# Kernel tuning notes

Hardware: AMD Instinct MI355X
Metric: run time of the kernel (lower is better)

## Reference

```python
import jax, jax.numpy as jnp
import numpy as np

WAY = 5
TEMPERATURE = 0.2
TEMPERATURE_ATTN = 5.0
BN_EPS = 1e-5


def bn_apply(x, p):
    # p: (4, C) = gamma, beta, running_mean, running_var (eval-mode BatchNorm)
    g, b, m, v = p[0], p[1], p[2], p[3]
    sh = (1, -1) + (1,) * (x.ndim - 2)
    return (x - m.reshape(sh)) * (g.reshape(sh) / jnp.sqrt(v.reshape(sh) + BN_EPS)) + b.reshape(sh)


def conv3d(x, w, pad):
    return jax.lax.conv_general_dilated(
        x, w, (1, 1, 1), [(pad[0], pad[0]), (pad[1], pad[1]), (pad[2], pad[2])],
        dimension_numbers=('NCDHW', 'OIDHW', 'NCDHW'))


def sepconv4d(x, conv2_w, bn2, conv1_w, bn1, proj_w, bnp):
    # x: (b, c, u, v, h, w). conv2: (k,k,1) kernel over (u,v); conv1: (1,k,k) over (h,w).
    b, c, u, v, h, w = x.shape
    y = x.reshape(b, c, u, v, h * w)
    y = bn_apply(conv3d(y, conv2_w, (1, 1, 0)), bn2)
    y = jax.nn.relu(y)
    y = y.reshape(b, c, u * v, h, w)
    y = bn_apply(conv3d(y, conv1_w, (0, 1, 1)), bn1)
    # 1x1 projection (pointwise over channels) + BN
    y = jnp.einsum('oc,bcxhw->boxhw', proj_w, y)
    y = bn_apply(y, bnp)
    return y.reshape(b, -1, u, v, h, w)


def cca(x, c1, c2):
    def branch(z):
        z = sepconv4d(z, *c1)
        z = jax.nn.relu(z)
        z = sepconv4d(z, *c2)
        return z
    perm = (0, 1, 4, 5, 2, 3)
    return branch(x) + jnp.transpose(branch(jnp.transpose(x, perm)), perm)


def gaussian_normalize(x, axis, eps=1e-5):
    m = jnp.mean(x, axis=axis, keepdims=True)
    v = jnp.var(x, axis=axis, keepdims=True, ddof=1)  # torch.var is unbiased
    return (x - m) / jnp.sqrt(v + eps)


def setup_inputs() -> dict:
    key = jax.random.key(0)
    ks = jax.random.split(key, 16)

    def bn_params(k, c):
        k1, k2, k3, k4 = jax.random.split(k, 4)
        g = 1.0 + 0.1 * jax.random.normal(k1, (c,), jnp.float32)
        b = 0.1 * jax.random.normal(k2, (c,), jnp.float32)
        m = 0.1 * jax.random.normal(k3, (c,), jnp.float32)
        v = 1.0 + 0.1 * jax.random.uniform(k4, (c,), jnp.float32)
        return jnp.stack([g, b, m, v])

    return {
        'spt': jax.random.normal(ks[0], (1, 5, 640, 10, 10), jnp.float32),
        'qry': jax.random.normal(ks[1], (75, 640, 10, 10), jnp.float32),
        'w_1x1': jax.random.normal(ks[2], (64, 640), jnp.float32) * 0.04,
        'bn_1x1': bn_params(ks[3], 64),
        'c1_conv2_w': jax.random.normal(ks[4], (1, 1, 3, 3, 1), jnp.float32) * 0.33,
        'c1_bn2': bn_params(ks[5], 1),
        'c1_conv1_w': jax.random.normal(ks[6], (1, 1, 1, 3, 3), jnp.float32) * 0.33,
        'c1_bn1': bn_params(ks[7], 1),
        'c1_proj_w': jax.random.normal(ks[8], (16, 1), jnp.float32),
        'c1_bnp': bn_params(ks[9], 16),
        'c2_conv2_w': jax.random.normal(ks[10], (16, 16, 3, 3, 1), jnp.float32) * 0.083,
        'c2_bn2': bn_params(ks[11], 16),
        'c2_conv1_w': jax.random.normal(ks[12], (16, 16, 1, 3, 3), jnp.float32) * 0.083,
        'c2_bn1': bn_params(ks[13], 16),
        'c2_proj_w': jax.random.normal(ks[14], (1, 16), jnp.float32) * 0.25,
        'c2_bnp': bn_params(ks[15], 1),
    }


def reference(spt, qry, w_1x1, bn_1x1,
              c1_conv2_w, c1_bn2, c1_conv1_w, c1_bn1, c1_proj_w, c1_bnp,
              c2_conv2_w, c2_bn2, c2_conv1_w, c2_bn1, c2_proj_w, c2_bnp):
    s = spt[0]                                   # (way, C, H, W)
    s = s - s.mean(axis=1, keepdims=True)        # normalize_feature
    q = qry - qry.mean(axis=1, keepdims=True)

    def cca1x1(x):
        y = jnp.einsum('oc,bchw->bohw', w_1x1, x)
        return jax.nn.relu(bn_apply(y, bn_1x1))

    sf = cca1x1(s)
    qf = cca1x1(q)
    sf = sf / jnp.maximum(jnp.linalg.norm(sf, axis=1, keepdims=True), 1e-8)
    qf = qf / jnp.maximum(jnp.linalg.norm(qf, axis=1, keepdims=True), 1e-8)

    # 4D correlation (avoids the repeat-induced 6D blowup of the original)
    corr = jnp.einsum('ncij,qckl->qnijkl', sf, qf)  # (Q, way, Hs, Ws, Hq, Wq)
    Q, way, Hs, Ws, Hq, Wq = corr.shape

    c1 = (c1_conv2_w, c1_bn2, c1_conv1_w, c1_bn1, c1_proj_w, c1_bnp)
    c2 = (c2_conv2_w, c2_bn2, c2_conv1_w, c2_bn1, c2_proj_w, c2_bnp)
    corr = cca(corr.reshape(Q * way, 1, Hs, Ws, Hq, Wq), c1, c2)

    corr_s = corr.reshape(Q, way, Hs * Ws, Hq, Wq)
    corr_q = corr.reshape(Q, way, Hs, Ws, Hq * Wq)
    corr_s = gaussian_normalize(corr_s, axis=2)
    corr_q = gaussian_normalize(corr_q, axis=4)
    corr_s = jax.nn.softmax(corr_s / TEMPERATURE_ATTN, axis=2).reshape(Q, way, Hs, Ws, Hq, Wq)
    corr_q = jax.nn.softmax(corr_q / TEMPERATURE_ATTN, axis=4).reshape(Q, way, Hs, Ws, Hq, Wq)

    attn_s = corr_s.sum(axis=(4, 5))             # (Q, way, Hs, Ws)
    attn_q = corr_q.sum(axis=(2, 3))             # (Q, way, Hq, Wq)

    spt_att = (attn_s[:, :, None] * s[None]).mean(axis=(-1, -2))       # (Q, way, C)
    qry_att = (attn_q[:, :, None] * q[:, None]).mean(axis=(-1, -2))    # (Q, way, C)
    qry_pooled = q.mean(axis=(-1, -2))                                  # (Q, C)

    num = jnp.sum(spt_att * qry_att, axis=-1)
    den = (jnp.maximum(jnp.linalg.norm(spt_att, axis=-1), 1e-8) *
           jnp.maximum(jnp.linalg.norm(qry_att, axis=-1), 1e-8))
    sim = (num / den) / TEMPERATURE
    return sim, qry_pooled
```

## Files before the change

### kernel.cpp

```cpp
#include <hip/hip_runtime.h>


#define NITEM 375

#define OFF_XTS 0
#define OFF_XTQ 160000
#define OFF_MP  2560000
#define OFF_SF  2568000
#define OFF_QF  2600000
#define OFF_RA  3080000
#define OFF_RB  6830000
#define OFF_PRM 10655000

#define PK2F 232
#define PK1F 1512
#define WSUMF 2792
#define SCVF 2856
#define SHVF 2920
#define PKWF 2984

#define Y1SLOT0  23680
#define Y1GAP3   3200
#define Y1SSTR3  35200
#define ZPB3     20480
#define Y2S3     129280
#define LDS_TOTAL3 161536

typedef float f4v __attribute__((ext_vector_type(4)));
typedef float f32x4 __attribute__((ext_vector_type(4)));
typedef _Float16 half8v __attribute__((ext_vector_type(8)));
typedef __fp16 fp16x2 __attribute__((ext_vector_type(2)));
typedef unsigned int u32x4 __attribute__((ext_vector_type(4)));
typedef unsigned int u32x2 __attribute__((ext_vector_type(2)));

__device__ __forceinline__ unsigned int pkrtz(float a, float b) {
  union { fp16x2 h; unsigned int u; } cv;
  cv.h = __builtin_amdgcn_cvt_pkrtz(a, b);
  return cv.u;
}

__global__ __launch_bounds__(256) void k_prep(
    const float* __restrict__ w1x1,  const float* __restrict__ bn1x1,
    const float* __restrict__ c1c2w, const float* __restrict__ c1bn2,
    const float* __restrict__ c1c1w, const float* __restrict__ c1bn1,
    const float* __restrict__ c1pj,  const float* __restrict__ c1bnp,
    const float* __restrict__ c2c2w, const float* __restrict__ c2bn2,
    const float* __restrict__ c2c1w, const float* __restrict__ c2bn1,
    const float* __restrict__ c2pj,  const float* __restrict__ c2bnp,
    float* __restrict__ prm)
{
  (void)w1x1; (void)bn1x1;
  const int t = threadIdx.x;
  const float eps = 1e-5f;

  for (int idx = t; idx < 144; idx += 256) {
    int ds = idx / 16, i = idx % 16;
    float spv = c2bnp[0] / sqrtf(c2bnp[3] + eps);
    float acc = 0.f;
    for (int o = 0; o < 16; ++o) {
      float s1 = c2bn1[o] / sqrtf(c2bn1[48 + o] + eps);
      acc += c2pj[o] * s1 * c2c1w[(o * 16 + i) * 9 + ds];
    }
    prm[idx] = spv * acc;
  }
  for (int i = t; i < 16; i += 256) {
    float s = c1bnp[i] / sqrtf(c1bnp[48 + i] + eps);
    prm[144 + i] = s * c1pj[i];
    prm[160 + i] = c1bnp[16 + i] - c1bnp[32 + i] * s;
  }
  for (int o = t; o < 16; o += 256) {
    float s = c2bn2[o] / sqrtf(c2bn2[48 + o] + eps);
    prm[176 + o] = s;
    prm[192 + o] = c2bn2[16 + o] - c2bn2[32 + o] * s;
  }
  for (int k = t; k < 9; k += 256) {
    prm[208 + k] = c1c2w[k];
    prm[217 + k] = c1c1w[k];
  }
  if (t == 0) {
    float S2 = c1bn2[0] / sqrtf(c1bn2[3] + eps);
    prm[226] = S2;
    prm[227] = c1bn2[1] - c1bn2[2] * S2;
    float S1 = c1bn1[0] / sqrtf(c1bn1[3] + eps);
    prm[228] = S1;
    prm[229] = c1bn1[1] - c1bn1[2] * S1;
    float spv = c2bnp[0] / sqrtf(c2bnp[3] + eps);
    float k0 = 0.f;
    for (int o = 0; o < 16; ++o) {
      float s1 = c2bn1[o] / sqrtf(c2bn1[48 + o] + eps);
      k0 += c2pj[o] * (c2bn1[16 + o] - c2bn1[32 + o] * s1);
    }
    prm[230] = spv * (k0 - c2bnp[2]) + c2bnp[1];
    prm[231] = 0.f;
  }
  __syncthreads();

  _Float16* pk2 = (_Float16*)(prm + PK2F);
  for (int idx = t; idx < 2560; idx += 256) {
    int c = idx >> 9, rem = idx & 511;
    int ln = rem >> 3, j = rem & 7;
    int o = ln & 15, qq = ln >> 4;
    int tap = 2 * c + (qq >> 1);
    int i = (qq & 1) * 8 + j;
    float v = (tap < 9) ? c2c2w[(o * 16 + i) * 9 + tap] : 0.f;
    pk2[idx] = (_Float16)v;
  }
  _Float16* pk1 = (_Float16*)(prm + PK1F);
  for (int idx = t; idx < 2560; idx += 256) {
    int c = idx >> 9, rem = idx & 511;
    int ln = rem >> 3, j = rem & 7;
    int m = ln & 15, qq = ln >> 4;
    int k = c * 32 + qq * 8 + j;
    int tp = k >> 4, i = k & 15;
    float v = (m == 0 && tp < 9) ? prm[tp * 16 + i] : 0.f;
    pk1[idx] = (_Float16)v;
  }
}

__global__ __launch_bounds__(256) void k_prepw(
    const float* __restrict__ w1x1, const float* __restrict__ bn1x1,
    float* __restrict__ prm)
{
  __shared__ float red[4];
  _Float16* pkw = (_Float16*)(prm + PKWF);
  const int t = threadIdx.x;
  const int base = blockIdx.x * 800;
  for (int r = t; r < 800; r += 256) {
    int idx = base + r;
    int fi = idx >> 9, rem = idx & 511;
    int ln = rem >> 3, j = rem & 7;
    int cc = fi / 10, r2 = fi - cc * 10;
    int mt = r2 >> 1, kk = r2 & 1;
    int m = mt * 16 + (ln & 15);
    int k = cc * 64 + kk * 32 + ((ln >> 4) & 3) * 8 + j;
    float v = (m < 64) ? w1x1[m * 640 + k] : (m == 64 ? 1.f : 0.f);
    pkw[idx] = (_Float16)v;
  }
  const int o = blockIdx.x;
  float s = 0.f;
  for (int c = t; c < 640; c += 256) s += w1x1[o * 640 + c];
  #pragma unroll
  for (int off = 32; off > 0; off >>= 1) s += __shfl_down(s, off);
  if ((t & 63) == 0) red[t >> 6] = s;
  __syncthreads();
  if (t == 0) {
    prm[WSUMF + o] = red[0] + red[1] + red[2] + red[3];
    float scv = bn1x1[o] / sqrtf(bn1x1[192 + o] + 1e-5f);
    prm[SCVF + o] = scv;
    prm[SHVF + o] = bn1x1[64 + o] - bn1x1[128 + o] * scv;
  }
}

__global__ __launch_bounds__(512) void k_feat(
    const float* __restrict__ spt, const float* __restrict__ qry,
    float* __restrict__ ws, float* __restrict__ out)
{
  __shared__ __align__(16) char POOL[2 * 16128];
  __shared__ __align__(16) float mrow[112];
  __shared__ __align__(16) float rn[112];
  __shared__ float CS[2][512];
  __shared__ float RS[640];
  __shared__ float msumL;

  const int b = blockIdx.x, t = threadIdx.x;
  const int lane = t & 63, wvv = t >> 6;
  const int n0 = lane & 15, qd = (lane >> 4) & 3;
  const float* src = (b < 5) ? spt + b * 64000 : qry + (b - 5) * 64000;
  float* dst = (b < 5) ? ws + OFF_SF + b * 6400 : ws + OFF_QF + (b - 5) * 6400;
  unsigned int* xtg = (unsigned int*)(ws + ((b < 5) ? (OFF_XTS + b * 32000)
                                                    : (OFF_XTQ + (b - 5) * 32000)));
  const float* prm = ws + OFF_PRM;
  const _Float16* pkw = (const _Float16*)(prm + PKWF);

  for (int idx = t; idx < 864; idx += 512) {
    int bsel = idx / 432, r = idx - bsel * 432;
    ((unsigned int*)(POOL + bsel * 16128 + 100 * 144))[r] = 0u;
  }
  for (int u = t; u < 800; u += 512) {
    int cp = u / 25, p4 = u - cp * 25;
    const float* r0 = src + (2 * cp) * 100 + p4 * 4;
    f4v a = *(const f4v*)r0;
    f4v c1 = *(const f4v*)(r0 + 100);
    #pragma unroll
    for (int e = 0; e < 4; ++e)
      *(unsigned int*)((_Float16*)POOL + (p4 * 4 + e) * 72 + 2 * cp) = pkrtz(a[e], c1[e]);
  }
  __syncthreads();

  const int chp = t >> 3, part = t & 7;
  const int pLo = part * 13, pHi = (pLo + 13 < 100) ? pLo + 13 : 100;

  f32x4 acc[5];
  #pragma unroll
  for (int ti = 0; ti < 5; ++ti) { acc[ti][0]=0.f; acc[ti][1]=0.f; acc[ti][2]=0.f; acc[ti][3]=0.f; }

  for (int cc = 0; cc < 10; ++cc) {
    const int cur = cc & 1;
    const _Float16* Xc = (const _Float16*)(POOL + cur * 16128);
    _Float16* Xn = (_Float16*)(POOL + (cur ^ 1) * 16128);

    f4v pa[2], pc[2];
    if (cc < 9) {
      #pragma unroll
      for (int k = 0; k < 2; ++k) {
        int u = t + k * 512;
        if (u < 800) {
          int cp = u / 25, p4 = u - cp * 25;
          const float* r0 = src + ((cc + 1) * 64 + 2 * cp) * 100 + p4 * 4;
          pa[k] = *(const f4v*)r0;
          pc[k] = *(const f4v*)(r0 + 100);
        }
      }
    }
    for (int u = t; u < 3200; u += 512) {
      int p = u >> 5, cp = u & 31;
      xtg[p * 320 + cc * 32 + cp] = *(const unsigned int*)(Xc + p * 72 + 2 * cp);
    }
    #pragma unroll
    for (int kk = 0; kk < 2; ++kk) {
      #pragma unroll
      for (int ti = 0; ti < 5; ++ti) {
        int idx = wvv + ti * 8; if (idx > 34) idx = 34;
        int mt = idx / 7, nt = idx - mt * 7;
        half8v av = *(const half8v*)(pkw + (cc * 10 + mt * 2 + kk) * 512 + lane * 8);
        half8v bv = *(const half8v*)(Xc + (nt * 16 + n0) * 72 + kk * 32 + qd * 8);
        acc[ti] = __builtin_amdgcn_mfma_f32_16x16x32_f16(av, bv, acc[ti], 0, 0, 0);
      }
    }
    {
      float s = 0.f;
      for (int p = pLo; p < pHi; ++p) s += (float)Xc[p * 72 + chp];
      CS[cur][t] = s;
    }
    if (cc < 9) {
      #pragma unroll
      for (int k = 0; k < 2; ++k) {
        int u = t + k * 512;
        if (u < 800) {
          int cp = u / 25, p4 = u - cp * 25;
          #pragma unroll
          for (int e = 0; e < 4; ++e)
            *(unsigned int*)(Xn + (p4 * 4 + e) * 72 + 2 * cp) = pkrtz(pa[k][e], pc[k][e]);
        }
      }
    }
    __syncthreads();
    if (t < 64) {
      float s = 0.f;
      #pragma unroll
      for (int k = 0; k < 8; ++k) s += CS[cur][t * 8 + k];
      RS[cc * 64 + t] = s;
    }
  }
  #pragma unroll
  for (int ti = 0; ti < 5; ++ti) {
    int idx = wvv + ti * 8; if (idx > 34) idx = 34;
    int mt = idx / 7, nt = idx - mt * 7;
    if (mt == 4 && qd == 0) {
      int p = nt * 16 + n0;
      mrow[p] = acc[ti][0] * (1.f / 640.f);
    }
  }
  __syncthreads();
  float* OUT = (float*)POOL;
  if (t == 0) { float s = 0.f; for (int p = 0; p < 100; ++p) s += mrow[p]; msumL = s; }
  #pragma unroll
  for (int ti = 0; ti < 5; ++ti) {
    int idx = wvv + ti * 8; if (idx > 34) idx = 34;
    int mt = idx / 7, nt = idx - mt * 7;
    if (mt < 4) {
      int p = nt * 16 + n0;
      if (p < 100) {
        float mp = mrow[p];
        #pragma unroll
        for (int r = 0; r < 4; ++r) {
          int o = mt * 16 + qd * 4 + r;
          float v = acc[ti][r] - prm[WSUMF + o] * mp;
          v = prm[SCVF + o] * v + prm[SHVF + o];
          OUT[o * 104 + p] = v > 0.f ? v : 0.f;
        }
      }
    }
  }
  __syncthreads();
  if (t < 100) {
    float s = 0.f;
    for (int o = 0; o < 64; ++o) { float v = OUT[o * 104 + t]; s += v * v; }
    float nr = sqrtf(s);
    rn[t] = 1.f / (nr > 1e-8f ? nr : 1e-8f);
    ws[OFF_MP + b * 100 + t] = mrow[t];
  }
  __syncthreads();
  for (int idx = t; idx < 1600; idx += 512) {
    int o = idx / 25, pq = idx - o * 25;
    f4v v = *(const f4v*)(OUT + o * 104 + pq * 4);
    f4v r4 = *(const f4v*)(rn + pq * 4);
    #pragma unroll
    for (int e = 0; e < 4; ++e) v[e] *= r4[e];
    *(f4v*)(dst + o * 100 + pq * 4) = v;
  }
  if (b >= 5) {
    const float msum = msumL;
    for (int gc = t; gc < 640; gc += 512)
      out[375 + (b - 5) * 640 + gc] = (RS[gc] - msum) * 0.01f;
  }
}

__global__ __launch_bounds__(1024) __attribute__((amdgpu_waves_per_eu(4, 4)))
void k_cca(float* __restrict__ ws)
{
  extern __shared__ char smem[];
  _Float16* T2h = (_Float16*)smem;
  float* sfL  = (float*)(smem + 20480);
  float* qfL  = (float*)(smem + 46080);
  float* CORR = (float*)(smem + 71680);
  float* T1   = (float*)(smem + 20480);

  const float* prm = ws + OFF_PRM;
  const int bid = blockIdx.x;
  const int it = bid >> 1, br = bid & 1;
  const int q = it / 5, n = it % 5;
  const int t = threadIdx.x;
  const int lane = t & 63, wv = t >> 6;
  const int n0 = lane & 15, qd = (lane >> 4) & 3;
  const int qh = qd >> 1, ih = qd & 1;

  const _Float16* pk2 = (const _Float16*)(prm + PK2F);
  const _Float16* pk1 = (const _Float16*)(prm + PK1F);
  half8v A2[5], A1[5];
  #pragma unroll
  for (int c = 0; c < 5; ++c) {
    A2[c] = *(const half8v*)(pk2 + c * 512 + lane * 8);
    A1[c] = *(const half8v*)(pk1 + c * 512 + lane * 8);
  }
  float sc2[4], bc2[4];
  #pragma unroll
  for (int r = 0; r < 4; ++r) { sc2[r] = prm[176 + qd * 4 + r]; bc2[r] = prm[192 + qd * 4 + r]; }

  const int d1E[5] = {-1,-1, 0, 0, 1}, d2E[5] = {-1, 1, 0,-1, 1};
  const int d1O[5] = {-1, 0, 0, 1, 0}, d2O[5] = { 0,-1, 1, 0, 0};

  int pp1[4], st1[4], addr2[4][5], posB[4];
  bool pv[4];
  #pragma unroll
  for (int ti = 0; ti < 4; ++ti) {
    int tile = wv + ti * 16; if (tile > 62) tile = 62;
    const int p = tile * 16 + n0;
    const int pcp = p < 1000 ? p : 999;
    pp1[ti] = pcp * 32 + ih * 16;
    st1[ti] = Y2S3 + p * 32 + qh * 16 + ih * 8;
    pv[ti] = (qd == 0) && (p < 1000);
    const int f2 = pcp / 100;
    const int s = pcp - f2 * 100;
    const int s1 = s / 10, s2 = s - s1 * 10;
    const bool rm = s1 > 0, rp = s1 < 9, cm = s2 > 0, cp2 = s2 < 9;
    const int b0 = Y2S3 + pcp * 32 + ih * 16;
    #pragma unroll
    for (int c = 0; c < 5; ++c) {
      const bool vE = (d1E[c] < 0 ? rm : (d1E[c] > 0 ? rp : true)) &&
                      (d2E[c] < 0 ? cm : (d2E[c] > 0 ? cp2 : true));
      const bool vO = (c == 4) ? false :
                      ((d1O[c] < 0 ? rm : (d1O[c] > 0 ? rp : true)) &&
                       (d2O[c] < 0 ? cm : (d2O[c] > 0 ? cp2 : true)));
      const bool v = qh ? vO : vE;
      const int D1c = (qh ? (d1O[c] * 10 + d2O[c]) : (d1E[c] * 10 + d2E[c]));
      addr2[ti][c] = v ? (b0 + D1c * 32) : ZPB3;
    }
    posB[ti] = br ? (s * 100 + f2) : (f2 * 100 + s);
  }
  const int posStride = br ? 10 : 1000;

  {
    const f4v* sf4 = (const f4v*)(ws + OFF_SF + n * 6400);
    const f4v* qf4 = (const f4v*)(ws + OFF_QF + q * 6400);
    f4v* sL4 = (f4v*)sfL; f4v* qL4 = (f4v*)qfL;
    for (int idx = t; idx < 1600; idx += 1024) { sL4[idx] = sf4[idx]; qL4[idx] = qf4[idx]; }
  }
  __syncthreads();

  if (t < 625) {
    const int ij0 = (t / 25) * 4, kl0 = (t % 25) * 4;
    f4v acc4[4];
    #pragma unroll
    for (int jj = 0; jj < 4; ++jj) { acc4[jj][0]=0.f; acc4[jj][1]=0.f; acc4[jj][2]=0.f; acc4[jj][3]=0.f; }
    for (int c = 0; c < 64; ++c) {
      f4v sv = *(const f4v*)(sfL + c * 100 + ij0);
      f4v qv = *(const f4v*)(qfL + c * 100 + kl0);
      #pragma unroll
      for (int jj = 0; jj < 4; ++jj)
        #pragma unroll
        for (int e = 0; e < 4; ++e) acc4[jj][e] += sv[jj] * qv[e];
    }
    if (br == 0) {
      #pragma unroll
      for (int jj = 0; jj < 4; ++jj) *(f4v*)(CORR + (ij0 + jj) * 100 + kl0) = acc4[jj];
    } else {
      #pragma unroll
      for (int kk = 0; kk < 4; ++kk) {
        f4v tr;
        #pragma unroll
        for (int jj = 0; jj < 4; ++jj) tr[jj] = acc4[jj][kk];
        *(f4v*)(CORR + (kl0 + kk) * 100 + ij0) = tr;
      }
    }
  }
  __syncthreads();

  const float S2 = prm[226], B2 = prm[227], S1 = prm[228], B1 = prm[229];

  for (int idx = t; idx < 2500; idx += 1024) {
    int f = idx / 25, sq = (idx % 25) * 4;
    int f1 = f / 10, f2 = f - f1 * 10;
    f4v acc; acc[0]=0.f; acc[1]=0.f; acc[2]=0.f; acc[3]=0.f;
    #pragma unroll
    for (int du = 0; du < 3; ++du) {
      int nf1 = f1 + du - 1;
      if ((unsigned)nf1 >= 10u) continue;
      #pragma unroll
      for (int dv = 0; dv < 3; ++dv) {
        int nf2 = f2 + dv - 1;
        if ((unsigned)nf2 >= 10u) continue;
        float w = prm[208 + du * 3 + dv];
        f4v xv = *(const f4v*)(CORR + (nf1 * 10 + nf2) * 100 + sq);
        #pragma unroll
        for (int e = 0; e < 4; ++e) acc[e] += w * xv[e];
      }
    }
    #pragma unroll
    for (int e = 0; e < 4; ++e) { float v = S2 * acc[e] + B2; acc[e] = v > 0.f ? v : 0.f; }
    *(f4v*)(T1 + f * 100 + sq) = acc;
  }
  __syncthreads();

  if (t < 1000) {
    const int f = t / 10, s1 = t - (t / 10) * 10;
    const float* rowB = T1 + f * 100;
    f4v r[3][3];
    float w[3][3];
    #pragma unroll
    for (int dh = 0; dh < 3; ++dh) {
      int rr = s1 + dh - 1;
      bool okr = (unsigned)rr < 10u;
      int rc = rr < 0 ? 0 : (rr > 9 ? 9 : rr);
      const float* rp = rowB + rc * 10;
      r[dh][0] = *(const f4v*)(rp);
      r[dh][1] = *(const f4v*)(rp + 4);
      r[dh][2] = *(const f4v*)(rp + 8);
      #pragma unroll
      for (int dw = 0; dw < 3; ++dw) w[dh][dw] = okr ? prm[217 + dh * 3 + dw] : 0.f;
    }
    float o[10];
    #pragma unroll
    for (int s2 = 0; s2 < 10; ++s2) {
      float a = 0.f;
      #pragma unroll
      for (int dh = 0; dh < 3; ++dh)
        #pragma unroll
        for (int dw = 0; dw < 3; ++dw) {
          int col = s2 + dw - 1;
          if (col < 0 || col > 9) continue;
          a += w[dh][dw] * r[dh][col >> 2][col & 3];
        }
      o[s2] = a;
    }
    unsigned int* dst = (unsigned int*)((char*)T2h + (f * 100 + s1 * 10) * 2);
    #pragma unroll
    for (int k = 0; k < 5; ++k)
      dst[k] = pkrtz(S1 * o[2 * k] + B1, S1 * o[2 * k + 1] + B1);
  }
  __syncthreads();

  #define GEN_Y1(F1N)                                                          \
    if (t < 1000) {                                                            \
      const int _sl = (F1N) % 3;                                               \
      const float t2 = (float)T2h[(F1N) * 1000 + t];                           \
      unsigned int d[8];                                                       \
      _Pragma("unroll")                                                        \
      for (int j = 0; j < 8; ++j) {                                            \
        float ya = fmaxf(prm[144 + 2 * j] * t2 + prm[160 + 2 * j], 0.f);       \
        float yb = fmaxf(prm[145 + 2 * j] * t2 + prm[161 + 2 * j], 0.f);       \
        d[j] = pkrtz(ya, yb);                                                  \
      }                                                                        \
      u32x4 lo, hi;                                                            \
      lo[0]=d[0]; lo[1]=d[1]; lo[2]=d[2]; lo[3]=d[3];                          \
      hi[0]=d[4]; hi[1]=d[5]; hi[2]=d[6]; hi[3]=d[7];                          \
      *(u32x4*)(smem + Y1SLOT0 + _sl * Y1SSTR3 + t * 32) = lo;                 \
      *(u32x4*)(smem + Y1SLOT0 + _sl * Y1SSTR3 + t * 32 + 16) = hi;            \
    }

  GEN_Y1(0)
  GEN_Y1(1)
  {
    u32x4 zz; zz[0] = 0u; zz[1] = 0u; zz[2] = 0u; zz[3] = 0u;
    for (int idx = t; idx < 800; idx += 1024) {
      const int r = idx / 200;
      *(u32x4*)(smem + 20480 + r * Y1SSTR3 + (idx - r * 200) * 16) = zz;
    }
    for (int idx = t; idx < 2000; idx += 1024)
      *(u32x4*)(smem + Y1SLOT0 + 2 * Y1SSTR3 + idx * 16) = zz;
  }
  __syncthreads();

  const float Cf = prm[230];
  float* resb = ws + (br ? OFF_RB : OFF_RA) + it * 10000;
  int gp = 0;

  for (int g = 0; g < 10; ++g) {
    const int o0 = (g % 3) * Y1SSTR3;
    const int oP = ((g + 1) % 3) * Y1SSTR3;
    const int oM = ((g + 2) % 3) * Y1SSTR3;
    int base1[5];
    #pragma unroll
    for (int c = 0; c < 5; ++c) {
      const int eb = (d1E[c] < 0 ? oM : (d1E[c] > 0 ? oP : o0)) + d2E[c] * 3200;
      const int ob = (d1O[c] < 0 ? oM : (d1O[c] > 0 ? oP : o0)) + d2O[c] * 3200;
      base1[c] = Y1SLOT0 + (qh ? ob : eb);
    }

    #pragma unroll
    for (int ti = 0; ti < 4; ++ti) {
      f32x4 acc; acc[0]=0.f; acc[1]=0.f; acc[2]=0.f; acc[3]=0.f;
      #pragma unroll
      for (int c = 0; c < 5; ++c) {
        half8v b = *(const half8v*)(smem + base1[c] + pp1[ti]);
        acc = __builtin_amdgcn_mfma_f32_16x16x32_f16(A2[c], b, acc, 0, 0, 0);
      }
      const float v0 = fmaxf(sc2[0] * acc[0] + bc2[0], 0.f);
      const float v1 = fmaxf(sc2[1] * acc[1] + bc2[1], 0.f);
      const float v2 = fmaxf(sc2[2] * acc[2] + bc2[2], 0.f);
      const float v3 = fmaxf(sc2[3] * acc[3] + bc2[3], 0.f);
      u32x2 wq; wq[0] = pkrtz(v0, v1); wq[1] = pkrtz(v2, v3);
      *(u32x2*)(smem + st1[ti]) = wq;
    }
    __syncthreads();

    #pragma unroll
    for (int ti = 0; ti < 4; ++ti) {
      f32x4 acc; acc[0]=0.f; acc[1]=0.f; acc[2]=0.f; acc[3]=0.f;
      #pragma unroll
      for (int c = 0; c < 5; ++c) {
        half8v b = *(const half8v*)(smem + addr2[ti][c]);
        acc = __builtin_amdgcn_mfma_f32_16x16x32_f16(A1[c], b, acc, 0, 0, 0);
      }
      if (pv[ti]) resb[posB[ti] + gp] = acc[0] + Cf;
    }
    if (g + 2 <= 9) { GEN_Y1(g + 2) }
    else if (g == 8) {
      u32x4 zz; zz[0] = 0u; zz[1] = 0u; zz[2] = 0u; zz[3] = 0u;
      for (int idx = t; idx < 2000; idx += 1024)
        *(u32x4*)(smem + Y1SLOT0 + Y1SSTR3 + idx * 16) = zz;
    }
    gp += posStride;
    __syncthreads();
  }
  #undef GEN_Y1
}

__global__ __launch_bounds__(256) void k_post(float* __restrict__ ws,
                                              float* __restrict__ out)
{
  __shared__ float F[10000];
  __shared__ float mc[100], ic[100], rc[100];
  __shared__ float mr[100], ir[100], rr[100];
  __shared__ float asL[100], aqL[100], msL[100], mqL[100];
  __shared__ float alph[2];
  __shared__ float red[12];
  const int it = blockIdx.x, t = threadIdx.x;
  const int q = it / 5, n = it % 5;

  const f4v* ra4 = (const f4v*)(ws + OFF_RA + it * 10000);
  const f4v* rb4 = (const f4v*)(ws + OFF_RB + it * 10000);
  f4v* F4 = (f4v*)F;
  for (int idx = t; idx < 2500; idx += 256) {
    f4v a = ra4[idx], b = rb4[idx];
    #pragma unroll
    for (int e = 0; e < 4; ++e) a[e] += b[e];
    F4[idx] = a;
  }
  if (t < 100) msL[t] = ws[OFF_MP + n * 100 + t];
  else if (t < 200) mqL[t - 100] = ws[OFF_MP + (5 + q) * 100 + t - 100];
  __syncthreads();

  if (t < 100) {
    float s = 0.f;
    for (int ij = 0; ij < 100; ++ij) s += F[ij * 100 + t];
    float m = s * 0.01f;
    float ss = 0.f;
    for (int ij = 0; ij < 100; ++ij) { float d = F[ij * 100 + t] - m; ss += d * d; }
    float inv = 1.f / (sqrtf(ss * (1.f / 99.f) + 1e-5f) * 5.f);
    float den = 0.f;
    for (int ij = 0; ij < 100; ++ij) den += __expf((F[ij * 100 + t] - m) * inv);
    mc[t] = m; ic[t] = inv; rc[t] = 1.f / den;
  } else if (t < 200) {
    const int r = t - 100;
    float s = 0.f;
    for (int kl = 0; kl < 100; ++kl) s += F[r * 100 + kl];
    float m = s * 0.01f;
    float ss = 0.f;
    for (int kl = 0; kl < 100; ++kl) { float d = F[r * 100 + kl] - m; ss += d * d; }
    float inv = 1.f / (sqrtf(ss * (1.f / 99.f) + 1e-5f) * 5.f);
    float den = 0.f;
    for (int kl = 0; kl < 100; ++kl) den += __expf((F[r * 100 + kl] - m) * inv);
    mr[r] = m; ir[r] = inv; rr[r] = 1.f / den;
  }
  __syncthreads();
  if (t < 100) {
    float s = 0.f;
    for (int kl = 0; kl < 100; ++kl)
      s += __expf((F[t * 100 + kl] - mc[kl]) * ic[kl]) * rc[kl];
    asL[t] = s;
  } else if (t < 200) {
    const int r = t - 100;
    float s2 = 0.f;
    for (int ij = 0; ij < 100; ++ij)
      s2 += __expf((F[ij * 100 + r] - mr[ij]) * ir[ij]) * rr[ij];
    aqL[r] = s2;
  }
  __syncthreads();
  if (t < 2) {
    float s = 0.f;
    for (int p = 0; p < 100; ++p) s += t ? (aqL[p] * mqL[p]) : (asL[p] * msL[p]);
    alph[t] = s;
  }
  __syncthreads();

  const unsigned int* xs = (const unsigned int*)(ws + OFF_XTS + n * 32000);
  const unsigned int* xq = (const unsigned int*)(ws + OFF_XTQ + q * 32000);
  const float als = alph[0], alq = alph[1];
  float dot = 0.f, na = 0.f, nb = 0.f;
  for (int u = t; u < 320; u += 256) {
    float s0 = 0.f, s1 = 0.f, q0 = 0.f, q1 = 0.f;
    for (int p = 0; p < 100; ++p) {
      union { unsigned int u; fp16x2 h; } a, bq;
      a.u = xs[p * 320 + u];
      bq.u = xq[p * 320 + u];
      float ap = asL[p], qp = aqL[p];
      s0 += ap * (float)a.h[0]; s1 += ap * (float)a.h[1];
      q0 += qp * (float)bq.h[0]; q1 += qp * (float)bq.h[1];
    }
    float sa0 = (s0 - als) * 0.01f, sa1 = (s1 - als) * 0.01f;
    float qa0 = (q0 - alq) * 0.01f, qa1 = (q1 - alq) * 0.01f;
    dot += sa0 * qa0 + sa1 * qa1;
    na  += sa0 * sa0 + sa1 * sa1;
    nb  += qa0 * qa0 + qa1 * qa1;
  }
  #pragma unroll
  for (int off = 32; off > 0; off >>= 1) {
    dot += __shfl_down(dot, off);
    na  += __shfl_down(na, off);
    nb  += __shfl_down(nb, off);
  }
  const int wid = t >> 6, lanei = t & 63;
  if (lanei == 0) { red[wid * 3 + 0] = dot; red[wid * 3 + 1] = na; red[wid * 3 + 2] = nb; }
  __syncthreads();
  if (t == 0) {
    dot = red[0] + red[3] + red[6] + red[9];
    na  = red[1] + red[4] + red[7] + red[10];
    nb  = red[2] + red[5] + red[8] + red[11];
    float ns = sqrtf(na); ns = ns > 1e-8f ? ns : 1e-8f;
    float nq2 = sqrtf(nb); nq2 = nq2 > 1e-8f ? nq2 : 1e-8f;
    out[it] = dot / (ns * nq2) * 5.f;
  }
}

extern "C" void kernel_launch(void* const* d_in, const int* in_sizes, int n_in,
                              void* d_out, int out_size, void* d_ws, size_t ws_size,
                              hipStream_t stream)
{
  (void)in_sizes; (void)n_in; (void)out_size; (void)ws_size;
  const float* spt    = (const float*)d_in[0];
  const float* qry    = (const float*)d_in[1];
  const float* w1x1   = (const float*)d_in[2];
  const float* bn1x1  = (const float*)d_in[3];
  const float* c1c2w  = (const float*)d_in[4];
  const float* c1bn2  = (const float*)d_in[5];
  const float* c1c1w  = (const float*)d_in[6];
  const float* c1bn1  = (const float*)d_in[7];
  const float* c1pj   = (const float*)d_in[8];
  const float* c1bnp  = (const float*)d_in[9];
  const float* c2c2w  = (const float*)d_in[10];
  const float* c2bn2  = (const float*)d_in[11];
  const float* c2c1w  = (const float*)d_in[12];
  const float* c2bn1  = (const float*)d_in[13];
  const float* c2pj   = (const float*)d_in[14];
  const float* c2bnp  = (const float*)d_in[15];
  float* ws  = (float*)d_ws;
  float* out = (float*)d_out;

  k_prep<<<1, 256, 0, stream>>>(w1x1, bn1x1,
                                c1c2w, c1bn2, c1c1w, c1bn1, c1pj, c1bnp,
                                c2c2w, c2bn2, c2c1w, c2bn1, c2pj, c2bnp,
                                ws + OFF_PRM);
  k_prepw<<<64, 256, 0, stream>>>(w1x1, bn1x1, ws + OFF_PRM);
  k_feat<<<80, 512, 0, stream>>>(spt, qry, ws, out);

  (void)hipFuncSetAttribute((const void*)k_cca,
                            hipFuncAttributeMaxDynamicSharedMemorySize, LDS_TOTAL3);
  k_cca<<<NITEM * 2, 1024, LDS_TOTAL3, stream>>>(ws);

  k_post<<<NITEM, 256, 0, stream>>>(ws, out);
}
```

Baseline: 329.0 us.

## Compute correlation with fp16 MFMA from prepacked features and padded CORR layout

The feature kernel now writes normalized features as packed fp16 pairs in an MFMA operand layout instead of fp32 rows. The CCA kernel then computes the 100x100 correlation with 16x16x32 f16 MFMA instructions straight from global memory, replacing the LDS staging and the scalar FMA loop. CORR and T1 switch to a padded 12-wide row stride. The first (u,v) conv is restructured so each thread sweeps 7 input rows and produces 5 outputs, reusing loaded values. This trades fp32 precision in the correlation for matrix-core throughput and fewer LDS loads.

Result: faster. 312.1 us, median of 3 (-5.2%).

```diff
diff --git a/kernel.cpp b/kernel.cpp
--- a/kernel.cpp
+++ b/kernel.cpp
@@ -166,7 +166,6 @@
   const int lane = t & 63, wvv = t >> 6;
   const int n0 = lane & 15, qd = (lane >> 4) & 3;
   const float* src = (b < 5) ? spt + b * 64000 : qry + (b - 5) * 64000;
-  float* dst = (b < 5) ? ws + OFF_SF + b * 6400 : ws + OFF_QF + (b - 5) * 6400;
   unsigned int* xtg = (unsigned int*)(ws + ((b < 5) ? (OFF_XTS + b * 32000)
                                                     : (OFF_XTQ + (b - 5) * 32000)));
   const float* prm = ws + OFF_PRM;
@@ -291,13 +290,24 @@
     ws[OFF_MP + b * 100 + t] = mrow[t];
   }
   __syncthreads();
-  for (int idx = t; idx < 1600; idx += 512) {
-    int o = idx / 25, pq = idx - o * 25;
-    f4v v = *(const f4v*)(OUT + o * 104 + pq * 4);
-    f4v r4 = *(const f4v*)(rn + pq * 4);
-    #pragma unroll
-    for (int e = 0; e < 4; ++e) v[e] *= r4[e];
-    *(f4v*)(dst + o * 100 + pq * 4) = v;
+  {
+    unsigned int* fg = (unsigned int*)((b < 5) ? (ws + OFF_SF) : (ws + OFF_QF))
+                       + ((b < 5) ? b : (b - 5)) * 3584;
+    for (int idx = t; idx < 3584; idx += 512) {
+      const int jj = idx & 3;
+      const int ln2 = (idx >> 2) & 63;
+      const int fi = idx >> 8;
+      const int kk = fi / 7, pt = fi - kk * 7;
+      const int pos = pt * 16 + (ln2 & 15);
+      const int c0 = kk * 32 + ((ln2 >> 4) & 3) * 8 + 2 * jj;
+      float a = 0.f, bb = 0.f;
+      if (pos < 100) {
+        const float rv = rn[pos];
+        a = OUT[c0 * 104 + pos] * rv;
+        bb = OUT[(c0 + 1) * 104 + pos] * rv;
+      }
+      fg[idx] = pkrtz(a, bb);
+    }
   }
   if (b >= 5) {
     const float msum = msumL;
@@ -311,10 +321,8 @@
 {
   extern __shared__ char smem[];
   _Float16* T2h = (_Float16*)smem;
-  float* sfL  = (float*)(smem + 20480);
-  float* qfL  = (float*)(smem + 46080);
+  float* T1   = (float*)(smem + 20480);
   float* CORR = (float*)(smem + 71680);
-  float* T1   = (float*)(smem + 20480);
 
   const float* prm = ws + OFF_PRM;
   const int bid = blockIdx.x;
@@ -371,70 +379,77 @@
   const int posStride = br ? 10 : 1000;
 
   {
-    const f4v* sf4 = (const f4v*)(ws + OFF_SF + n * 6400);
-    const f4v* qf4 = (const f4v*)(ws + OFF_QF + q * 6400);
-    f4v* sL4 = (f4v*)sfL; f4v* qL4 = (f4v*)qfL;
-    for (int idx = t; idx < 1600; idx += 1024) { sL4[idx] = sf4[idx]; qL4[idx] = qf4[idx]; }
-  }
-  __syncthreads();
-
-  if (t < 625) {
-    const int ij0 = (t / 25) * 4, kl0 = (t % 25) * 4;
-    f4v acc4[4];
-    #pragma unroll
-    for (int jj = 0; jj < 4; ++jj) { acc4[jj][0]=0.f; acc4[jj][1]=0.f; acc4[jj][2]=0.f; acc4[jj][3]=0.f; }
-    for (int c = 0; c < 64; ++c) {
-      f4v sv = *(const f4v*)(sfL + c * 100 + ij0);
-      f4v qv = *(const f4v*)(qfL + c * 100 + kl0);
-      #pragma unroll
-      for (int jj = 0; jj < 4; ++jj)
+    const half8v* fS = (const half8v*)(ws + OFF_SF) + n * 896;
+    const half8v* fQ = (const half8v*)(ws + OFF_QF) + q * 896;
+    const half8v* FA = br ? fQ : fS;
+    const half8v* FB = br ? fS : fQ;
+    #pragma unroll
+    for (int ti = 0; ti < 4; ++ti) {
+      int T = wv + ti * 16; if (T > 48) T = 48;
+      const int mt = T / 7, nt = T - mt * 7;
+      half8v a0 = FA[mt * 64 + lane];
+      half8v b0 = FB[nt * 64 + lane];
+      half8v a1 = FA[(7 + mt) * 64 + lane];
+      half8v b1 = FB[(7 + nt) * 64 + lane];
+      f32x4 acc; acc[0]=0.f; acc[1]=0.f; acc[2]=0.f; acc[3]=0.f;
+      acc = __builtin_amdgcn_mfma_f32_16x16x32_f16(a0, b0, acc, 0, 0, 0);
+      acc = __builtin_amdgcn_mfma_f32_16x16x32_f16(a1, b1, acc, 0, 0, 0);
+      const int s = nt * 16 + n0;
+      if (s < 100) {
+        const int s1a = s / 10;
+        float* cp0 = CORR + s1a * 12 + (s - s1a * 10);
+        const int r0 = mt * 16 + qd * 4;
         #pragma unroll
-        for (int e = 0; e < 4; ++e) acc4[jj][e] += sv[jj] * qv[e];
-    }
-    if (br == 0) {
-      #pragma unroll
-      for (int jj = 0; jj < 4; ++jj) *(f4v*)(CORR + (ij0 + jj) * 100 + kl0) = acc4[jj];
-    } else {
-      #pragma unroll
-      for (int kk = 0; kk < 4; ++kk) {
-        f4v tr;
+        for (int r = 0; r < 4; ++r)
+          if (r0 + r < 100) cp0[(r0 + r) * 120] = acc[r];
+      }
+    }
+  }
+  __syncthreads();
+
+  const float S2 = prm[226], B2 = prm[227], S1 = prm[228], B1 = prm[229];
+
+  if (t < 600) {
+    const int h = t / 300, r2 = t - h * 300;
+    const int f2 = r2 / 30, r3 = r2 - f2 * 30;
+    const int s1v = r3 / 3, s2q = r3 - s1v * 3;
+    const int cb = s1v * 12 + s2q * 4;
+    f4v outv[5];
+    #pragma unroll
+    for (int i = 0; i < 5; ++i) { outv[i][0]=0.f; outv[i][1]=0.f; outv[i][2]=0.f; outv[i][3]=0.f; }
+    #pragma unroll
+    for (int k = 0; k < 7; ++k) {
+      const int nf1 = 5 * h - 1 + k;
+      if ((unsigned)nf1 >= 10u) continue;
+      #pragma unroll
+      for (int dv = 0; dv < 3; ++dv) {
+        const int nf2 = f2 + dv - 1;
+        if ((unsigned)nf2 >= 10u) continue;
+        f4v x = *(const f4v*)(CORR + (nf1 * 10 + nf2) * 120 + cb);
         #pragma unroll
-        for (int jj = 0; jj < 4; ++jj) tr[jj] = acc4[jj][kk];
-        *(f4v*)(CORR + (kl0 + kk) * 100 + ij0) = tr;
-      }
-    }
-  }
-  __syncthreads();
-
-  const float S2 = prm[226], B2 = prm[227], S1 = prm[228], B1 = prm[229];
-
-  for (int idx = t; idx < 2500; idx += 1024) {
-    int f = idx / 25, sq = (idx % 25) * 4;
-    int f1 = f / 10, f2 = f - f1 * 10;
-    f4v acc; acc[0]=0.f; acc[1]=0.f; acc[2]=0.f; acc[3]=0.f;
-    #pragma unroll
-    for (int du = 0; du < 3; ++du) {
-      int nf1 = f1 + du - 1;
-      if ((unsigned)nf1 >= 10u) continue;
-      #pragma unroll
-      for (int dv = 0; dv < 3; ++dv) {
-        int nf2 = f2 + dv - 1;
-        if ((unsigned)nf2 >= 10u) continue;
-        float w = prm[208 + du * 3 + dv];
-        f4v xv = *(const f4v*)(CORR + (nf1 * 10 + nf2) * 100 + sq);
-        #pragma unroll
-        for (int e = 0; e < 4; ++e) acc[e] += w * xv[e];
-      }
-    }
-    #pragma unroll
-    for (int e = 0; e < 4; ++e) { float v = S2 * acc[e] + B2; acc[e] = v > 0.f ? v : 0.f; }
-    *(f4v*)(T1 + f * 100 + sq) = acc;
+        for (int du = 0; du < 3; ++du) {
+          const int f1l = k - du;
+          if (f1l < 0 || f1l > 4) continue;
+          const float w = prm[208 + du * 3 + dv];
+          #pragma unroll
+          for (int e = 0; e < 4; ++e) outv[f1l][e] += w * x[e];
+        }
+      }
+    }
+    #pragma unroll
+    for (int f1l = 0; f1l < 5; ++f1l) {
+      const int f = (5 * h + f1l) * 10 + f2;
+      f4v v;
+      #pragma unroll
+      for (int e = 0; e < 4; ++e) { float z = S2 * outv[f1l][e] + B2; v[e] = z > 0.f ? z : 0.f; }
+      *(f4v*)(T1 + f * 120 + cb) = v;
+    }
   }
   __syncthreads();
 
   if (t < 1000) {
     const int f = t / 10, s1 = t - (t / 10) * 10;
-    const float* rowB = T1 + f * 100;
+    const float* rowB = T1 + f * 120;
     f4v r[3][3];
     float w[3][3];
     #pragma unroll
@@ -442,7 +457,7 @@
       int rr = s1 + dh - 1;
       bool okr = (unsigned)rr < 10u;
       int rc = rr < 0 ? 0 : (rr > 9 ? 9 : rr);
-      const float* rp = rowB + rc * 10;
+      const float* rp = rowB + rc * 12;
       r[dh][0] = *(const f4v*)(rp);
       r[dh][1] = *(const f4v*)(rp + 4);
       r[dh][2] = *(const f4v*)(rp + 8);
```
